# Optimization experiments

Hardware: AMD Instinct MI355X
Metric: run time of the kernel (lower is better)

Reference implementation:

```python
import jax, jax.numpy as jnp
import numpy as np

N_NODES = 50000
N_EDGES = 800000
D = 256
N_LAYERS = 2


def setup_inputs() -> dict:
    key = jax.random.key(0)
    k1, k2, k3, k4, k5, k6 = jax.random.split(key, 6)
    inp = {}
    inp["input"] = jax.random.normal(k1, (N_NODES, D), dtype=jnp.float32)
    inp["edge_index"] = jax.random.randint(k2, (2, N_EDGES), 0, N_NODES, dtype=jnp.int64)
    # learned params: initial dense projection + per-conv GCN weights
    scale = 1.0 / np.sqrt(D)
    inp["weight"] = jax.random.normal(k3, (D, D), dtype=jnp.float32) * scale
    inp["bias"] = jnp.zeros((D,), dtype=jnp.float32)
    inp["conv_w"] = jax.random.normal(k4, (N_LAYERS, D, D), dtype=jnp.float32) * scale
    inp["conv_b"] = jnp.zeros((N_LAYERS, D), dtype=jnp.float32)
    return inp


def _gcn_conv(x, W, b, src, dst, n):
    # Standard GCNConv: x' = D^{-1/2} (A + I) D^{-1/2} (x W) + b
    h = x @ W  # [N, D]
    loops = jnp.arange(n, dtype=src.dtype)
    s = jnp.concatenate([src, loops])
    d = jnp.concatenate([dst, loops])
    deg = jax.ops.segment_sum(jnp.ones(s.shape[0], dtype=x.dtype), d, num_segments=n)
    dinv = jnp.where(deg > 0, deg ** -0.5, 0.0)
    norm = dinv[s] * dinv[d]  # [E+N]
    msg = h[s] * norm[:, None]  # gather + scale  [E+N, D]
    return jax.ops.segment_sum(msg, d, num_segments=n) + b  # scatter-add


def reference(input, edge_index, weight, bias, conv_w, conv_b):
    n = input.shape[0]
    src, dst = edge_index[0], edge_index[1]
    # dropout=0 / eval mode -> identity
    x = jax.nn.relu(input @ weight + bias)
    for i in range(conv_w.shape[0]):
        x = jax.nn.relu(_gcn_conv(x, conv_w[i], conv_b[i], src, dst, n))
    return x
```

## Files before the change

kernel.cpp:

```cpp
#include <hip/hip_runtime.h>

#define D 256
typedef unsigned short u16;
typedef __attribute__((ext_vector_type(8))) short bf16x8;
typedef __attribute__((ext_vector_type(4))) float f32x4;

__device__ __forceinline__ float bf2f(u16 u) {
    union { unsigned int i; float f; } x; x.i = ((unsigned int)u) << 16; return x.f;
}
__device__ __forceinline__ u16 f2bf(float f) {
    union { float f; unsigned int i; } x; x.f = f;
    unsigned int r = x.i + 0x7fff + ((x.i >> 16) & 1);
    return (u16)(r >> 16);
}
__device__ __forceinline__ unsigned int cvtpk_bf16(float lo, float hi) {
    unsigned int r;
    asm("v_cvt_pk_bf16_f32 %0, %1, %2" : "=v"(r) : "v"(lo), "v"(hi));
    return r;
}
__device__ __forceinline__ void gload16(const void* g, void* l) {
    __builtin_amdgcn_global_load_lds(
        (const __attribute__((address_space(1))) void*)g,
        (__attribute__((address_space(3))) void*)l, 16, 0, 0);
}
__device__ __forceinline__ bf16x8 gload_row(const u16* p) {
    bf16x8 r;
    asm volatile("global_load_dwordx4 %0, %1, off" : "=&v"(r) : "v"(p));
    return r;
}


__global__ void init_kernel(int* __restrict__ deg, int n) {
    int i = blockIdx.x * blockDim.x + threadIdx.x;
    if (i < n) deg[i] = 1;
}

__global__ void hist_kernel(const int* __restrict__ dst, int* __restrict__ deg, int e) {
    int i = blockIdx.x * blockDim.x + threadIdx.x;
    if (i < e) atomicAdd(&deg[dst[i]], 1);
}


__global__ __launch_bounds__(256) void scan_phase1(
    const int* __restrict__ deg, int* __restrict__ bsum,
    float* __restrict__ dinv, int n) {
    __shared__ int red[256];
    int t = threadIdx.x;
    int i0 = blockIdx.x * 1024 + t * 4;
    int s = 0;
    if (i0 + 3 < n) {
        int4 v = *reinterpret_cast<const int4*>(&deg[i0]);
        s = v.x + v.y + v.z + v.w - 4;
        float4 dv;
        dv.x = rsqrtf((float)v.x); dv.y = rsqrtf((float)v.y);
        dv.z = rsqrtf((float)v.z); dv.w = rsqrtf((float)v.w);
        *reinterpret_cast<float4*>(&dinv[i0]) = dv;
    } else {
        for (int j = i0; j < n && j < i0 + 4; ++j) {
            s += deg[j] - 1;
            dinv[j] = rsqrtf((float)deg[j]);
        }
    }
    red[t] = s;
    __syncthreads();
    for (int off = 128; off > 0; off >>= 1) {
        if (t < off) red[t] += red[t + off];
        __syncthreads();
    }
    if (t == 0) bsum[blockIdx.x] = red[0];
}

__global__ __launch_bounds__(256) void scan_phase2(
    const int* __restrict__ bsum, int* __restrict__ boff,
    int* __restrict__ rowptr, int nblk, int n) {
    __shared__ int sums[256];
    int t = threadIdx.x;
    int v = (t < nblk) ? bsum[t] : 0;
    int orig = v;
    sums[t] = v;
    __syncthreads();
    for (int off = 1; off < 256; off <<= 1) {
        int u = (t >= off) ? sums[t - off] : 0;
        __syncthreads();
        sums[t] += u;
        __syncthreads();
    }
    if (t < nblk) boff[t] = sums[t] - orig;
    if (t == nblk - 1) rowptr[n] = sums[t];
}

__global__ __launch_bounds__(256) void scan_phase3(
    const int* __restrict__ deg, const int* __restrict__ boff,
    int* __restrict__ rowptr, int* __restrict__ cursor, int n) {
    __shared__ int sums[256];
    int t = threadIdx.x;
    int i0 = blockIdx.x * 1024 + t * 4;
    int d0 = 0, d1 = 0, d2 = 0, d3 = 0;
    if (i0 + 3 < n) {
        int4 v = *reinterpret_cast<const int4*>(&deg[i0]);
        d0 = v.x - 1; d1 = v.y - 1; d2 = v.z - 1; d3 = v.w - 1;
    } else {
        if (i0 + 0 < n) d0 = deg[i0 + 0] - 1;
        if (i0 + 1 < n) d1 = deg[i0 + 1] - 1;
        if (i0 + 2 < n) d2 = deg[i0 + 2] - 1;
        if (i0 + 3 < n) d3 = deg[i0 + 3] - 1;
    }
    int ts = d0 + d1 + d2 + d3;
    sums[t] = ts;
    __syncthreads();
    for (int off = 1; off < 256; off <<= 1) {
        int u = (t >= off) ? sums[t - off] : 0;
        __syncthreads();
        sums[t] += u;
        __syncthreads();
    }
    int pre = boff[blockIdx.x] + sums[t] - ts;
    if (i0 + 0 < n) { rowptr[i0 + 0] = pre; cursor[i0 + 0] = pre; } pre += d0;
    if (i0 + 1 < n) { rowptr[i0 + 1] = pre; cursor[i0 + 1] = pre; } pre += d1;
    if (i0 + 2 < n) { rowptr[i0 + 2] = pre; cursor[i0 + 2] = pre; } pre += d2;
    if (i0 + 3 < n) { rowptr[i0 + 3] = pre; cursor[i0 + 3] = pre; }
}

__global__ void fill_kernel(const int* __restrict__ src, const int* __restrict__ dst,
                            int* __restrict__ cursor, int* __restrict__ csr, int e) {
    int i = blockIdx.x * blockDim.x + threadIdx.x;
    if (i < e) {
        int d = dst[i];
        int p = atomicAdd(&cursor[d], 1);
        csr[p] = src[i];
    }
}


__global__ __launch_bounds__(256) void transpose_cvt_kernel(
    const float* __restrict__ W, u16* __restrict__ Wt) {
    __shared__ float t[32][33];
    int bx = blockIdx.x * 32, by = blockIdx.y * 32;
    int tx = threadIdx.x & 31, ty = threadIdx.x >> 5;
#pragma unroll
    for (int i = 0; i < 32; i += 8)
        t[ty + i][tx] = W[(size_t)(bx + ty + i) * D + by + tx];
    __syncthreads();
#pragma unroll
    for (int i = 0; i < 32; i += 8)
        Wt[(size_t)(by + ty + i) * D + bx + tx] = f2bf(t[tx][ty + i]);
}


__global__ __launch_bounds__(256) void mfma_gemm(
    const u16* __restrict__ A, const u16* __restrict__ Bt,
    const float* __restrict__ dinv,
    u16* __restrict__ C, int M)
{
    __shared__ u16 As[64 * 32];
    __shared__ u16 Bs[128 * 32];
    const int tid = threadIdx.x;
    const int lane = tid & 63;
    const int wave = tid >> 6;
    const int wr = wave >> 1, wc = wave & 1;
    const int row0 = blockIdx.y * 64, col0 = blockIdx.x * 128;
    const int l16 = lane & 15, kg = lane >> 4;

    f32x4 acc[2][4] = {};

    for (int k0 = 0; k0 < D; k0 += 32) {
        {
            int r = tid >> 2, c = tid & 3;
            int csw = c ^ ((r >> 1) & 3);
            char* ldsbase_a = (char*)As + ((tid & ~63) << 4);
            int grow = row0 + r; if (grow >= M) grow = M - 1;
            gload16(&A[(size_t)grow * D + k0 + csw * 8], ldsbase_a);
        }
#pragma unroll
        for (int i = 0; i < 2; ++i) {
            int idx = i * 256 + tid;
            int r = idx >> 2, c = idx & 3;
            int csw = c ^ ((r >> 1) & 3);
            char* ldsbase_b = (char*)Bs + ((i * 256 + (tid & ~63)) << 4);
            gload16(&Bt[(size_t)(col0 + r) * D + k0 + csw * 8], ldsbase_b);
        }
        __syncthreads();
        bf16x8 af[2], bfr[4];
        int ksw = kg ^ ((l16 >> 1) & 3);
#pragma unroll
        for (int m = 0; m < 2; ++m)
            af[m] = *reinterpret_cast<const bf16x8*>(&As[(wr * 32 + m * 16 + l16) * 32 + ksw * 8]);
#pragma unroll
        for (int nn = 0; nn < 4; ++nn)
            bfr[nn] = *reinterpret_cast<const bf16x8*>(&Bs[(wc * 64 + nn * 16 + l16) * 32 + ksw * 8]);
#pragma unroll
        for (int m = 0; m < 2; ++m)
#pragma unroll
            for (int nn = 0; nn < 4; ++nn)
                acc[m][nn] = __builtin_amdgcn_mfma_f32_16x16x32_bf16(
                    af[m], bfr[nn], acc[m][nn], 0, 0, 0);
        __syncthreads();
    }

#pragma unroll
    for (int m = 0; m < 2; ++m) {
#pragma unroll
        for (int nn = 0; nn < 4; ++nn) {
            int gcol = col0 + wc * 64 + nn * 16 + l16;
#pragma unroll
            for (int j = 0; j < 4; ++j) {
                int grow = row0 + wr * 32 + m * 16 + kg * 4 + j;
                if (grow >= M) continue;
                C[(size_t)grow * D + gcol] = f2bf(acc[m][nn][j] * dinv[grow]);
            }
        }
    }
}

__global__ __launch_bounds__(256) void mfma_gemm_f32a(
    const float* __restrict__ A, const u16* __restrict__ Bt,
    const float* __restrict__ bias,
    u16* __restrict__ C, int M)
{
    __shared__ u16 As[64 * 32];
    __shared__ u16 Bs[128 * 32];
    const int tid = threadIdx.x;
    const int lane = tid & 63;
    const int wave = tid >> 6;
    const int wr = wave >> 1, wc = wave & 1;
    const int row0 = blockIdx.y * 64, col0 = blockIdx.x * 128;
    const int l16 = lane & 15, kg = lane >> 4;

    f32x4 acc[2][4] = {};

    for (int k0 = 0; k0 < D; k0 += 32) {
#pragma unroll
        for (int i = 0; i < 2; ++i) {
            int idx = i * 256 + tid;
            int r = idx >> 2, c = idx & 3;
            int csw = c ^ ((r >> 1) & 3);
            char* ldsbase_b = (char*)Bs + ((i * 256 + (tid & ~63)) << 4);
            gload16(&Bt[(size_t)(col0 + r) * D + k0 + csw * 8], ldsbase_b);
        }
        {
            int r = tid >> 2, c = tid & 3;
            int csw = c ^ ((r >> 1) & 3);
            int grow = row0 + r; if (grow >= M) grow = M - 1;
            const float* gp = &A[(size_t)grow * D + k0 + csw * 8];
            float4 v0 = *reinterpret_cast<const float4*>(gp);
            float4 v1 = *reinterpret_cast<const float4*>(gp + 4);
            uint4 w;
            w.x = cvtpk_bf16(v0.x, v0.y);
            w.y = cvtpk_bf16(v0.z, v0.w);
            w.z = cvtpk_bf16(v1.x, v1.y);
            w.w = cvtpk_bf16(v1.z, v1.w);
            *reinterpret_cast<uint4*>((char*)As + (tid << 4)) = w;
        }
        __syncthreads();
        bf16x8 af[2], bfr[4];
        int ksw = kg ^ ((l16 >> 1) & 3);
#pragma unroll
        for (int m = 0; m < 2; ++m)
            af[m] = *reinterpret_cast<const bf16x8*>(&As[(wr * 32 + m * 16 + l16) * 32 + ksw * 8]);
#pragma unroll
        for (int nn = 0; nn < 4; ++nn)
            bfr[nn] = *reinterpret_cast<const bf16x8*>(&Bs[(wc * 64 + nn * 16 + l16) * 32 + ksw * 8]);
#pragma unroll
        for (int m = 0; m < 2; ++m)
#pragma unroll
            for (int nn = 0; nn < 4; ++nn)
                acc[m][nn] = __builtin_amdgcn_mfma_f32_16x16x32_bf16(
                    af[m], bfr[nn], acc[m][nn], 0, 0, 0);
        __syncthreads();
    }

#pragma unroll
    for (int m = 0; m < 2; ++m) {
#pragma unroll
        for (int nn = 0; nn < 4; ++nn) {
            int gcol = col0 + wc * 64 + nn * 16 + l16;
#pragma unroll
            for (int j = 0; j < 4; ++j) {
                int grow = row0 + wr * 32 + m * 16 + kg * 4 + j;
                if (grow >= M) continue;
                C[(size_t)grow * D + gcol] = f2bf(fmaxf(acc[m][nn][j] + bias[gcol], 0.f));
            }
        }
    }
}

__global__ __launch_bounds__(256) void agg_kernel(
    const u16* __restrict__ hn, const int* __restrict__ rowptr,
    const int* __restrict__ csr, const float* __restrict__ dinv,
    const float* __restrict__ bias,
    u16* __restrict__ out_bf, float* __restrict__ out_f32, int n)
{
    int wave = threadIdx.x >> 6;
    int lane = threadIdx.x & 63;
    int node = blockIdx.x * 4 + wave;
    if (node >= n) return;
    int h = lane >> 5;
    int l5 = lane & 31;
    int c8 = l5 * 8;

    float a[8] = {0.f, 0.f, 0.f, 0.f, 0.f, 0.f, 0.f, 0.f};

#define ACC8(vv) { \
    a[0] += bf2f((u16)(vv)[0]); a[1] += bf2f((u16)(vv)[1]); \
    a[2] += bf2f((u16)(vv)[2]); a[3] += bf2f((u16)(vv)[3]); \
    a[4] += bf2f((u16)(vv)[4]); a[5] += bf2f((u16)(vv)[5]); \
    a[6] += bf2f((u16)(vv)[6]); a[7] += bf2f((u16)(vv)[7]); }
#define ROWP(s) (&hn[(size_t)(s) * D + c8])

    if (h == 0) {
        bf16x8 v = *reinterpret_cast<const bf16x8*>(ROWP(node));
        ACC8(v);
    }

    int e0 = rowptr[node], e1 = rowptr[node + 1];
    for (int base = e0; base < e1; base += 64) {
        int bi = base + lane;
        int idx = (bi < e1) ? csr[bi] : 0;
        int cnt = e1 - base; if (cnt > 64) cnt = 64;
        int it = 0;
        for (; it + 16 <= cnt; it += 16) {
            int s0 = __shfl(idx, it + 0  + h);
            int s1 = __shfl(idx, it + 2  + h);
            int s2 = __shfl(idx, it + 4  + h);
            int s3 = __shfl(idx, it + 6  + h);
            int s4 = __shfl(idx, it + 8  + h);
            int s5 = __shfl(idx, it + 10 + h);
            int s6 = __shfl(idx, it + 12 + h);
            int s7 = __shfl(idx, it + 14 + h);
            bf16x8 v0 = gload_row(ROWP(s0));
            bf16x8 v1 = gload_row(ROWP(s1));
            bf16x8 v2 = gload_row(ROWP(s2));
            bf16x8 v3 = gload_row(ROWP(s3));
            bf16x8 v4 = gload_row(ROWP(s4));
            bf16x8 v5 = gload_row(ROWP(s5));
            bf16x8 v6 = gload_row(ROWP(s6));
            bf16x8 v7 = gload_row(ROWP(s7));
            asm volatile("s_waitcnt vmcnt(0)" ::: "memory");
            __builtin_amdgcn_sched_barrier(0);
            ACC8(v0); ACC8(v1); ACC8(v2); ACC8(v3);
            ACC8(v4); ACC8(v5); ACC8(v6); ACC8(v7);
        }
        for (; it + 8 <= cnt; it += 8) {
            int s0 = __shfl(idx, it + 0 + h);
            int s1 = __shfl(idx, it + 2 + h);
            int s2 = __shfl(idx, it + 4 + h);
            int s3 = __shfl(idx, it + 6 + h);
            bf16x8 v0 = gload_row(ROWP(s0));
            bf16x8 v1 = gload_row(ROWP(s1));
            bf16x8 v2 = gload_row(ROWP(s2));
            bf16x8 v3 = gload_row(ROWP(s3));
            asm volatile("s_waitcnt vmcnt(0)" ::: "memory");
            __builtin_amdgcn_sched_barrier(0);
            ACC8(v0); ACC8(v1); ACC8(v2); ACC8(v3);
        }
        for (; it + 2 <= cnt; it += 2) {
            int s0 = __shfl(idx, it + h);
            bf16x8 v0 = *reinterpret_cast<const bf16x8*>(ROWP(s0));
            ACC8(v0);
        }
        if (it < cnt) {
            int s0 = __shfl(idx, it);
            if (h == 0) {
                bf16x8 v0 = *reinterpret_cast<const bf16x8*>(ROWP(s0));
                ACC8(v0);
            }
        }
    }
#undef ACC8
#undef ROWP

#pragma unroll
    for (int j = 0; j < 8; ++j) a[j] += __shfl(a[j], lane ^ 32);

    if (h == 0) {
        float di = dinv[node];
#pragma unroll
        for (int j = 0; j < 8; ++j) a[j] = fmaxf(a[j] * di + bias[c8 + j], 0.f);
        if (out_bf) {
            bf16x8 o;
#pragma unroll
            for (int j = 0; j < 8; ++j) o[j] = (short)f2bf(a[j]);
            *reinterpret_cast<bf16x8*>(&out_bf[(size_t)node * D + c8]) = o;
        } else {
            float4 o0, o1;
            o0.x = a[0]; o0.y = a[1]; o0.z = a[2]; o0.w = a[3];
            o1.x = a[4]; o1.y = a[5]; o1.z = a[6]; o1.w = a[7];
            *reinterpret_cast<float4*>(&out_f32[(size_t)node * D + c8 + 0]) = o0;
            *reinterpret_cast<float4*>(&out_f32[(size_t)node * D + c8 + 4]) = o1;
        }
    }
}


extern "C" void kernel_launch(void* const* d_in, const int* in_sizes, int n_in,
                              void* d_out, int out_size, void* d_ws, size_t ws_size,
                              hipStream_t stream) {
    const float* input  = (const float*)d_in[0];
    const int*   edge   = (const int*)d_in[1];
    const float* weight = (const float*)d_in[2];
    const float* bias   = (const float*)d_in[3];
    const float* conv_w = (const float*)d_in[4];
    const float* conv_b = (const float*)d_in[5];
    float* out = (float*)d_out;

    const int n = in_sizes[0] / D;
    const int E = in_sizes[1] / 2;
    const int* src = edge;
    const int* dst = edge + E;

    char* ws = (char*)d_ws;
    size_t off = 0;
    auto alloc = [&](size_t bytes) -> void* {
        void* p = ws + off;
        off = (off + bytes + 255) & ~(size_t)255;
        return p;
    };
    u16*   bufA   = (u16*)alloc((size_t)n * D * sizeof(u16));
    u16*   bufB   = (u16*)alloc((size_t)n * D * sizeof(u16));
    u16*   Wt     = (u16*)alloc((size_t)3 * D * D * sizeof(u16));
    int*   deg    = (int*)alloc((size_t)n * sizeof(int));
    int*   cursor = (int*)alloc((size_t)n * sizeof(int));
    float* dinv   = (float*)alloc((size_t)n * sizeof(float));
    int*   rowptr = (int*)alloc((size_t)(n + 1) * sizeof(int));
    int*   csr    = (int*)alloc((size_t)E * sizeof(int));
    int    nscan  = (n + 1023) / 1024;
    int*   bsum   = (int*)alloc((size_t)nscan * sizeof(int));
    int*   boff   = (int*)alloc((size_t)nscan * sizeof(int));

    int nb = (n + 255) / 256;
    int eb1 = (E + 255) / 256;
    init_kernel<<<nb, 256, 0, stream>>>(deg, n);
    hist_kernel<<<eb1, 256, 0, stream>>>(dst, deg, E);
    scan_phase1<<<nscan, 256, 0, stream>>>(deg, bsum, dinv, n);
    scan_phase2<<<1, 256, 0, stream>>>(bsum, boff, rowptr, nscan, n);
    scan_phase3<<<nscan, 256, 0, stream>>>(deg, boff, rowptr, cursor, n);
    fill_kernel<<<eb1, 256, 0, stream>>>(src, dst, cursor, csr, E);

    dim3 tgrid(8, 8);
    transpose_cvt_kernel<<<tgrid, 256, 0, stream>>>(weight, Wt);
    transpose_cvt_kernel<<<tgrid, 256, 0, stream>>>(conv_w, Wt + D * D);
    transpose_cvt_kernel<<<tgrid, 256, 0, stream>>>(conv_w + D * D, Wt + 2 * D * D);

    dim3 ggrid(D / 128, (n + 63) / 64);
    dim3 agrid((n + 3) / 4);

    mfma_gemm_f32a<<<ggrid, 256, 0, stream>>>(input, Wt, bias, bufA, n);
    mfma_gemm<<<ggrid, 256, 0, stream>>>(bufA, Wt + D * D, dinv, bufB, n);
    agg_kernel<<<agrid, 256, 0, stream>>>(bufB, rowptr, csr, dinv, conv_b, bufA, nullptr, n);
    mfma_gemm<<<ggrid, 256, 0, stream>>>(bufA, Wt + 2 * D * D, dinv, bufB, n);
    agg_kernel<<<agrid, 256, 0, stream>>>(bufB, rowptr, csr, dinv, conv_b + D, nullptr, out, n);
}
```

Measured before the change: 301.0 us.

## Merge independent graph-prep kernels into GEMM launches via block-index partitioning

Fuses the degree init with the weight transpose/convert, the degree histogram with the first dense GEMM, and the CSR fill with the first conv GEMM. Each merged launch splits its grid by block index so the graph-structure work runs alongside the GEMM tiles. This cuts launch count and lets the atomic-heavy, latency-bound passes fill idle CUs during compute. Dependencies still hold because the hist blocks do not touch GEMM1's inputs and dinv is ready before GEMM2. The risk is that atomic blocks contend for memory bandwidth with the GEMM tiles.

```diff
diff --git a/kernel.cpp b/kernel.cpp
--- a/kernel.cpp
+++ b/kernel.cpp
@@ -29,15 +29,31 @@
     return r;
 }
 
-
-__global__ void init_kernel(int* __restrict__ deg, int n) {
-    int i = blockIdx.x * blockDim.x + threadIdx.x;
-    if (i < n) deg[i] = 1;
-}
-
-__global__ void hist_kernel(const int* __restrict__ dst, int* __restrict__ deg, int e) {
-    int i = blockIdx.x * blockDim.x + threadIdx.x;
-    if (i < e) atomicAdd(&deg[dst[i]], 1);
+__global__ __launch_bounds__(256) void fused_init_tr(
+    int* __restrict__ deg, int n, int nb,
+    const float* __restrict__ W0, const float* __restrict__ CW,
+    u16* __restrict__ Wt)
+{
+    int bid = blockIdx.x;
+    if (bid < nb) {
+        int i = bid * 256 + threadIdx.x;
+        if (i < n) deg[i] = 1;
+    } else {
+        __shared__ float t[32][33];
+        int tt = bid - nb;
+        int w = tt >> 6, r = tt & 63;
+        const float* W = (w == 0) ? W0 : (CW + (size_t)(w - 1) * D * D);
+        u16* Wo = Wt + (size_t)w * D * D;
+        int bx = (r & 7) * 32, by = (r >> 3) * 32;
+        int tx = threadIdx.x & 31, ty = threadIdx.x >> 5;
+#pragma unroll
+        for (int i = 0; i < 32; i += 8)
+            t[ty + i][tx] = W[(size_t)(bx + ty + i) * D + by + tx];
+        __syncthreads();
+#pragma unroll
+        for (int i = 0; i < 32; i += 8)
+            Wo[(size_t)(by + ty + i) * D + bx + tx] = f2bf(t[tx][ty + i]);
+    }
 }
 
 
@@ -121,31 +137,159 @@
     if (i0 + 3 < n) { rowptr[i0 + 3] = pre; cursor[i0 + 3] = pre; }
 }
 
-__global__ void fill_kernel(const int* __restrict__ src, const int* __restrict__ dst,
-                            int* __restrict__ cursor, int* __restrict__ csr, int e) {
-    int i = blockIdx.x * blockDim.x + threadIdx.x;
-    if (i < e) {
-        int d = dst[i];
-        int p = atomicAdd(&cursor[d], 1);
-        csr[p] = src[i];
-    }
-}
-
-
-__global__ __launch_bounds__(256) void transpose_cvt_kernel(
-    const float* __restrict__ W, u16* __restrict__ Wt) {
-    __shared__ float t[32][33];
-    int bx = blockIdx.x * 32, by = blockIdx.y * 32;
-    int tx = threadIdx.x & 31, ty = threadIdx.x >> 5;
-#pragma unroll
-    for (int i = 0; i < 32; i += 8)
-        t[ty + i][tx] = W[(size_t)(bx + ty + i) * D + by + tx];
-    __syncthreads();
-#pragma unroll
-    for (int i = 0; i < 32; i += 8)
-        Wt[(size_t)(by + ty + i) * D + bx + tx] = f2bf(t[tx][ty + i]);
-}
-
+__global__ __launch_bounds__(256) void fused_gemm1_hist(
+    const float* __restrict__ A, const u16* __restrict__ Bt,
+    const float* __restrict__ bias, u16* __restrict__ C, int M, int ng,
+    const int* __restrict__ dst, int* __restrict__ deg, int E)
+{
+    int bid = blockIdx.x;
+    if (bid >= ng) {
+        int i = (bid - ng) * 256 + threadIdx.x;
+        if (i < E) atomicAdd(&deg[dst[i]], 1);
+        return;
+    }
+    __shared__ u16 As[64 * 32];
+    __shared__ u16 Bs[128 * 32];
+    const int tid = threadIdx.x;
+    const int lane = tid & 63;
+    const int wave = tid >> 6;
+    const int wr = wave >> 1, wc = wave & 1;
+    const int row0 = (bid >> 1) * 64, col0 = (bid & 1) * 128;
+    const int l16 = lane & 15, kg = lane >> 4;
+
+    f32x4 acc[2][4] = {};
+
+    for (int k0 = 0; k0 < D; k0 += 32) {
+#pragma unroll
+        for (int i = 0; i < 2; ++i) {
+            int idx = i * 256 + tid;
+            int r = idx >> 2, c = idx & 3;
+            int csw = c ^ ((r >> 1) & 3);
+            char* ldsbase_b = (char*)Bs + ((i * 256 + (tid & ~63)) << 4);
+            gload16(&Bt[(size_t)(col0 + r) * D + k0 + csw * 8], ldsbase_b);
+        }
+        {
+            int r = tid >> 2, c = tid & 3;
+            int csw = c ^ ((r >> 1) & 3);
+            int grow = row0 + r; if (grow >= M) grow = M - 1;
+            const float* gp = &A[(size_t)grow * D + k0 + csw * 8];
+            float4 v0 = *reinterpret_cast<const float4*>(gp);
+            float4 v1 = *reinterpret_cast<const float4*>(gp + 4);
+            uint4 w;
+            w.x = cvtpk_bf16(v0.x, v0.y);
+            w.y = cvtpk_bf16(v0.z, v0.w);
+            w.z = cvtpk_bf16(v1.x, v1.y);
+            w.w = cvtpk_bf16(v1.z, v1.w);
+            *reinterpret_cast<uint4*>((char*)As + (tid << 4)) = w;
+        }
+        __syncthreads();
+        bf16x8 af[2], bfr[4];
+        int ksw = kg ^ ((l16 >> 1) & 3);
+#pragma unroll
+        for (int m = 0; m < 2; ++m)
+            af[m] = *reinterpret_cast<const bf16x8*>(&As[(wr * 32 + m * 16 + l16) * 32 + ksw * 8]);
+#pragma unroll
+        for (int nn = 0; nn < 4; ++nn)
+            bfr[nn] = *reinterpret_cast<const bf16x8*>(&Bs[(wc * 64 + nn * 16 + l16) * 32 + ksw * 8]);
+#pragma unroll
+        for (int m = 0; m < 2; ++m)
+#pragma unroll
+            for (int nn = 0; nn < 4; ++nn)
+                acc[m][nn] = __builtin_amdgcn_mfma_f32_16x16x32_bf16(
+                    af[m], bfr[nn], acc[m][nn], 0, 0, 0);
+        __syncthreads();
+    }
+
+#pragma unroll
+    for (int m = 0; m < 2; ++m) {
+#pragma unroll
+        for (int nn = 0; nn < 4; ++nn) {
+            int gcol = col0 + wc * 64 + nn * 16 + l16;
+#pragma unroll
+            for (int j = 0; j < 4; ++j) {
+                int grow = row0 + wr * 32 + m * 16 + kg * 4 + j;
+                if (grow >= M) continue;
+                C[(size_t)grow * D + gcol] = f2bf(fmaxf(acc[m][nn][j] + bias[gcol], 0.f));
+            }
+        }
+    }
+}
+
+__global__ __launch_bounds__(256) void fused_gemm2_fill(
+    const u16* __restrict__ A, const u16* __restrict__ Bt,
+    const float* __restrict__ dinv, u16* __restrict__ C, int M, int ng,
+    const int* __restrict__ src, const int* __restrict__ dst,
+    int* __restrict__ cursor, int* __restrict__ csr, int E)
+{
+    int bid = blockIdx.x;
+    if (bid >= ng) {
+        int i = (bid - ng) * 256 + threadIdx.x;
+        if (i < E) {
+            int d = dst[i];
+            int p = atomicAdd(&cursor[d], 1);
+            csr[p] = src[i];
+        }
+        return;
+    }
+    __shared__ u16 As[64 * 32];
+    __shared__ u16 Bs[128 * 32];
+    const int tid = threadIdx.x;
+    const int lane = tid & 63;
+    const int wave = tid >> 6;
+    const int wr = wave >> 1, wc = wave & 1;
+    const int row0 = (bid >> 1) * 64, col0 = (bid & 1) * 128;
+    const int l16 = lane & 15, kg = lane >> 4;
+
+    f32x4 acc[2][4] = {};
+
+    for (int k0 = 0; k0 < D; k0 += 32) {
+        {
+            int r = tid >> 2, c = tid & 3;
+            int csw = c ^ ((r >> 1) & 3);
+            char* ldsbase_a = (char*)As + ((tid & ~63) << 4);
+            int grow = row0 + r; if (grow >= M) grow = M - 1;
+            gload16(&A[(size_t)grow * D + k0 + csw * 8], ldsbase_a);
+        }
+#pragma unroll
+        for (int i = 0; i < 2; ++i) {
+            int idx = i * 256 + tid;
+            int r = idx >> 2, c = idx & 3;
+            int csw = c ^ ((r >> 1) & 3);
+            char* ldsbase_b = (char*)Bs + ((i * 256 + (tid & ~63)) << 4);
+            gload16(&Bt[(size_t)(col0 + r) * D + k0 + csw * 8], ldsbase_b);
+        }
+        __syncthreads();
+        bf16x8 af[2], bfr[4];
+        int ksw = kg ^ ((l16 >> 1) & 3);
+#pragma unroll
+        for (int m = 0; m < 2; ++m)
+            af[m] = *reinterpret_cast<const bf16x8*>(&As[(wr * 32 + m * 16 + l16) * 32 + ksw * 8]);
+#pragma unroll
+        for (int nn = 0; nn < 4; ++nn)
+            bfr[nn] = *reinterpret_cast<const bf16x8*>(&Bs[(wc * 64 + nn * 16 + l16) * 32 + ksw * 8]);
+#pragma unroll
+        for (int m = 0; m < 2; ++m)
+#pragma unroll
+            for (int nn = 0; nn < 4; ++nn)
+                acc[m][nn] = __builtin_amdgcn_mfma_f32_16x16x32_bf16(
+                    af[m], bfr[nn], acc[m][nn], 0, 0, 0);
+        __syncthreads();
+    }
+
+#pragma unroll
+    for (int m = 0; m < 2; ++m) {
+#pragma unroll
+        for (int nn = 0; nn < 4; ++nn) {
+            int gcol = col0 + wc * 64 + nn * 16 + l16;
+#pragma unroll
+            for (int j = 0; j < 4; ++j) {
+                int grow = row0 + wr * 32 + m * 16 + kg * 4 + j;
+                if (grow >= M) continue;
+                C[(size_t)grow * D + gcol] = f2bf(acc[m][nn][j] * dinv[grow]);
+            }
+        }
+    }
+}
 
 __global__ __launch_bounds__(256) void mfma_gemm(
     const u16* __restrict__ A, const u16* __restrict__ Bt,
@@ -207,78 +351,6 @@
                 int grow = row0 + wr * 32 + m * 16 + kg * 4 + j;
                 if (grow >= M) continue;
                 C[(size_t)grow * D + gcol] = f2bf(acc[m][nn][j] * dinv[grow]);
-            }
-        }
-    }
-}
-
-__global__ __launch_bounds__(256) void mfma_gemm_f32a(
-    const float* __restrict__ A, const u16* __restrict__ Bt,
-    const float* __restrict__ bias,
-    u16* __restrict__ C, int M)
-{
-    __shared__ u16 As[64 * 32];
-    __shared__ u16 Bs[128 * 32];
-    const int tid = threadIdx.x;
-    const int lane = tid & 63;
-    const int wave = tid >> 6;
-    const int wr = wave >> 1, wc = wave & 1;
-    const int row0 = blockIdx.y * 64, col0 = blockIdx.x * 128;
-    const int l16 = lane & 15, kg = lane >> 4;
-
-    f32x4 acc[2][4] = {};
-
-    for (int k0 = 0; k0 < D; k0 += 32) {
-#pragma unroll
-        for (int i = 0; i < 2; ++i) {
-            int idx = i * 256 + tid;
-            int r = idx >> 2, c = idx & 3;
-            int csw = c ^ ((r >> 1) & 3);
-            char* ldsbase_b = (char*)Bs + ((i * 256 + (tid & ~63)) << 4);
-            gload16(&Bt[(size_t)(col0 + r) * D + k0 + csw * 8], ldsbase_b);
-        }
-        {
-            int r = tid >> 2, c = tid & 3;
-            int csw = c ^ ((r >> 1) & 3);
-            int grow = row0 + r; if (grow >= M) grow = M - 1;
-            const float* gp = &A[(size_t)grow * D + k0 + csw * 8];
-            float4 v0 = *reinterpret_cast<const float4*>(gp);
-            float4 v1 = *reinterpret_cast<const float4*>(gp + 4);
-            uint4 w;
-            w.x = cvtpk_bf16(v0.x, v0.y);
-            w.y = cvtpk_bf16(v0.z, v0.w);
-            w.z = cvtpk_bf16(v1.x, v1.y);
-            w.w = cvtpk_bf16(v1.z, v1.w);
-            *reinterpret_cast<uint4*>((char*)As + (tid << 4)) = w;
-        }
-        __syncthreads();
-        bf16x8 af[2], bfr[4];
-        int ksw = kg ^ ((l16 >> 1) & 3);
-#pragma unroll
-        for (int m = 0; m < 2; ++m)
-            af[m] = *reinterpret_cast<const bf16x8*>(&As[(wr * 32 + m * 16 + l16) * 32 + ksw * 8]);
-#pragma unroll
-        for (int nn = 0; nn < 4; ++nn)
-            bfr[nn] = *reinterpret_cast<const bf16x8*>(&Bs[(wc * 64 + nn * 16 + l16) * 32 + ksw * 8]);
-#pragma unroll
-        for (int m = 0; m < 2; ++m)
-#pragma unroll
-            for (int nn = 0; nn < 4; ++nn)
-                acc[m][nn] = __builtin_amdgcn_mfma_f32_16x16x32_bf16(
-                    af[m], bfr[nn], acc[m][nn], 0, 0, 0);
-        __syncthreads();
-    }
-
-#pragma unroll
-    for (int m = 0; m < 2; ++m) {
-#pragma unroll
-        for (int nn = 0; nn < 4; ++nn) {
-            int gcol = col0 + wc * 64 + nn * 16 + l16;
-#pragma unroll
-            for (int j = 0; j < 4; ++j) {
-                int grow = row0 + wr * 32 + m * 16 + kg * 4 + j;
-                if (grow >= M) continue;
-                C[(size_t)grow * D + gcol] = f2bf(fmaxf(acc[m][nn][j] + bias[gcol], 0.f));
             }
         }
     }
@@ -427,25 +499,20 @@
     int*   bsum   = (int*)alloc((size_t)nscan * sizeof(int));
     int*   boff   = (int*)alloc((size_t)nscan * sizeof(int));
 
-    int nb = (n + 255) / 256;
+    int nb  = (n + 255) / 256;
     int eb1 = (E + 255) / 256;
-    init_kernel<<<nb, 256, 0, stream>>>(deg, n);
-    hist_kernel<<<eb1, 256, 0, stream>>>(dst, deg, E);
+    int ng  = 2 * ((n + 63) / 64);
+
+    fused_init_tr<<<nb + 192, 256, 0, stream>>>(deg, n, nb, weight, conv_w, Wt);
+    fused_gemm1_hist<<<ng + eb1, 256, 0, stream>>>(input, Wt, bias, bufA, n, ng, dst, deg, E);
     scan_phase1<<<nscan, 256, 0, stream>>>(deg, bsum, dinv, n);
     scan_phase2<<<1, 256, 0, stream>>>(bsum, boff, rowptr, nscan, n);
     scan_phase3<<<nscan, 256, 0, stream>>>(deg, boff, rowptr, cursor, n);
-    fill_kernel<<<eb1, 256, 0, stream>>>(src, dst, cursor, csr, E);
-
-    dim3 tgrid(8, 8);
-    transpose_cvt_kernel<<<tgrid, 256, 0, stream>>>(weight, Wt);
-    transpose_cvt_kernel<<<tgrid, 256, 0, stream>>>(conv_w, Wt + D * D);
-    transpose_cvt_kernel<<<tgrid, 256, 0, stream>>>(conv_w + D * D, Wt + 2 * D * D);
+    fused_gemm2_fill<<<ng + eb1, 256, 0, stream>>>(bufA, Wt + D * D, dinv, bufB, n, ng,
+                                                   src, dst, cursor, csr, E);
 
     dim3 ggrid(D / 128, (n + 63) / 64);
     dim3 agrid((n + 3) / 4);
-
-    mfma_gemm_f32a<<<ggrid, 256, 0, stream>>>(input, Wt, bias, bufA, n);
-    mfma_gemm<<<ggrid, 256, 0, stream>>>(bufA, Wt + D * D, dinv, bufB, n);
     agg_kernel<<<agrid, 256, 0, stream>>>(bufB, rowptr, csr, dinv, conv_b, bufA, nullptr, n);
     mfma_gemm<<<ggrid, 256, 0, stream>>>(bufA, Wt + 2 * D * D, dinv, bufB, n);
     agg_kernel<<<agrid, 256, 0, stream>>>(bufB, rowptr, csr, dinv, conv_b + D, nullptr, out, n);
```

Result: faster. 294.8 us (-2.1%).

## Fuse degree init with weight transposes and first GEMM with histogram

Applied to the files above, without the earlier changes.

Merges the degree-init kernel and the three weight transpose/convert kernels into one launch, and runs the degree histogram as extra blocks of the first projection GEMM so the two overlap. The histogram and CSR fill kernels now process four edges per thread using int4 loads. This cuts six launches down to two and overlaps the atomic-heavy histogram with MFMA work. The cost is heterogeneous blocks competing for CU resources, plus a vectorized edge path that assumes 16-byte aligned src/dst arrays.

```diff
diff --git a/kernel.cpp b/kernel.cpp
--- a/kernel.cpp
+++ b/kernel.cpp
@@ -29,15 +29,31 @@
     return r;
 }
 
-
-__global__ void init_kernel(int* __restrict__ deg, int n) {
-    int i = blockIdx.x * blockDim.x + threadIdx.x;
-    if (i < n) deg[i] = 1;
-}
-
-__global__ void hist_kernel(const int* __restrict__ dst, int* __restrict__ deg, int e) {
-    int i = blockIdx.x * blockDim.x + threadIdx.x;
-    if (i < e) atomicAdd(&deg[dst[i]], 1);
+__global__ __launch_bounds__(256) void fused_init_tr(
+    int* __restrict__ deg, int n, int nb,
+    const float* __restrict__ W0, const float* __restrict__ CW,
+    u16* __restrict__ Wt)
+{
+    int bid = blockIdx.x;
+    if (bid < nb) {
+        int i = bid * 256 + threadIdx.x;
+        if (i < n) deg[i] = 1;
+    } else {
+        __shared__ float t[32][33];
+        int tt = bid - nb;
+        int w = tt >> 6, r = tt & 63;
+        const float* W = (w == 0) ? W0 : (CW + (size_t)(w - 1) * D * D);
+        u16* Wo = Wt + (size_t)w * D * D;
+        int bx = (r & 7) * 32, by = (r >> 3) * 32;
+        int tx = threadIdx.x & 31, ty = threadIdx.x >> 5;
+#pragma unroll
+        for (int i = 0; i < 32; i += 8)
+            t[ty + i][tx] = W[(size_t)(bx + ty + i) * D + by + tx];
+        __syncthreads();
+#pragma unroll
+        for (int i = 0; i < 32; i += 8)
+            Wo[(size_t)(by + ty + i) * D + bx + tx] = f2bf(t[tx][ty + i]);
+    }
 }
 
 
@@ -124,28 +140,108 @@
 __global__ void fill_kernel(const int* __restrict__ src, const int* __restrict__ dst,
                             int* __restrict__ cursor, int* __restrict__ csr, int e) {
     int i = blockIdx.x * blockDim.x + threadIdx.x;
-    if (i < e) {
-        int d = dst[i];
-        int p = atomicAdd(&cursor[d], 1);
-        csr[p] = src[i];
-    }
-}
-
-
-__global__ __launch_bounds__(256) void transpose_cvt_kernel(
-    const float* __restrict__ W, u16* __restrict__ Wt) {
-    __shared__ float t[32][33];
-    int bx = blockIdx.x * 32, by = blockIdx.y * 32;
-    int tx = threadIdx.x & 31, ty = threadIdx.x >> 5;
-#pragma unroll
-    for (int i = 0; i < 32; i += 8)
-        t[ty + i][tx] = W[(size_t)(bx + ty + i) * D + by + tx];
-    __syncthreads();
-#pragma unroll
-    for (int i = 0; i < 32; i += 8)
-        Wt[(size_t)(by + ty + i) * D + bx + tx] = f2bf(t[tx][ty + i]);
-}
-
+    int b = i * 4;
+    if (b + 3 < e) {
+        int4 s4 = *reinterpret_cast<const int4*>(&src[b]);
+        int4 d4 = *reinterpret_cast<const int4*>(&dst[b]);
+        int p;
+        p = atomicAdd(&cursor[d4.x], 1); csr[p] = s4.x;
+        p = atomicAdd(&cursor[d4.y], 1); csr[p] = s4.y;
+        p = atomicAdd(&cursor[d4.z], 1); csr[p] = s4.z;
+        p = atomicAdd(&cursor[d4.w], 1); csr[p] = s4.w;
+    } else {
+        for (int j = b; j < e; ++j) {
+            int d = dst[j];
+            int p = atomicAdd(&cursor[d], 1);
+            csr[p] = src[j];
+        }
+    }
+}
+
+__global__ __launch_bounds__(256) void fused_gemm1_hist(
+    const float* __restrict__ A, const u16* __restrict__ Bt,
+    const float* __restrict__ bias, u16* __restrict__ C, int M, int ng,
+    const int* __restrict__ dst, int* __restrict__ deg, int E)
+{
+    int bid = blockIdx.x;
+    if (bid >= ng) {
+        int i = (bid - ng) * 256 + threadIdx.x;
+        int b = i * 4;
+        if (b + 3 < E) {
+            int4 v = *reinterpret_cast<const int4*>(&dst[b]);
+            atomicAdd(&deg[v.x], 1); atomicAdd(&deg[v.y], 1);
+            atomicAdd(&deg[v.z], 1); atomicAdd(&deg[v.w], 1);
+        } else {
+            for (int j = b; j < E; ++j) atomicAdd(&deg[dst[j]], 1);
+        }
+        return;
+    }
+    __shared__ u16 As[64 * 32];
+    __shared__ u16 Bs[128 * 32];
+    const int tid = threadIdx.x;
+    const int lane = tid & 63;
+    const int wave = tid >> 6;
+    const int wr = wave >> 1, wc = wave & 1;
+    const int row0 = (bid >> 1) * 64, col0 = (bid & 1) * 128;
+    const int l16 = lane & 15, kg = lane >> 4;
+
+    f32x4 acc[2][4] = {};
+
+    for (int k0 = 0; k0 < D; k0 += 32) {
+#pragma unroll
+        for (int i = 0; i < 2; ++i) {
+            int idx = i * 256 + tid;
+            int r = idx >> 2, c = idx & 3;
+            int csw = c ^ ((r >> 1) & 3);
+            char* ldsbase_b = (char*)Bs + ((i * 256 + (tid & ~63)) << 4);
+            gload16(&Bt[(size_t)(col0 + r) * D + k0 + csw * 8], ldsbase_b);
+        }
+        {
+            int r = tid >> 2, c = tid & 3;
+            int csw = c ^ ((r >> 1) & 3);
+            int grow = row0 + r; if (grow >= M) grow = M - 1;
+            const float* gp = &A[(size_t)grow * D + k0 + csw * 8];
+            float4 v0 = *reinterpret_cast<const float4*>(gp);
+            float4 v1 = *reinterpret_cast<const float4*>(gp + 4);
+            uint4 w;
+            w.x = cvtpk_bf16(v0.x, v0.y);
+            w.y = cvtpk_bf16(v0.z, v0.w);
+            w.z = cvtpk_bf16(v1.x, v1.y);
+            w.w = cvtpk_bf16(v1.z, v1.w);
+            *reinterpret_cast<uint4*>((char*)As + (tid << 4)) = w;
+        }
+        __syncthreads();
+        bf16x8 af[2], bfr[4];
+        int ksw = kg ^ ((l16 >> 1) & 3);
+#pragma unroll
+        for (int m = 0; m < 2; ++m)
+            af[m] = *reinterpret_cast<const bf16x8*>(&As[(wr * 32 + m * 16 + l16) * 32 + ksw * 8]);
+#pragma unroll
+        for (int nn = 0; nn < 4; ++nn)
+            bfr[nn] = *reinterpret_cast<const bf16x8*>(&Bs[(wc * 64 + nn * 16 + l16) * 32 + ksw * 8]);
+#pragma unroll
+        for (int m = 0; m < 2; ++m)
+#pragma unroll
+            for (int nn = 0; nn < 4; ++nn)
+                acc[m][nn] = __builtin_amdgcn_mfma_f32_16x16x32_bf16(
+                    af[m], bfr[nn], acc[m][nn], 0, 0, 0);
+        __syncthreads();
+    }
+
+#pragma unroll
+    for (int m = 0; m < 2; ++m) {
+#pragma unroll
+        for (int nn = 0; nn < 4; ++nn) {
+            int gcol = col0 + wc * 64 + nn * 16 + l16;
+#pragma unroll
+            for (int j = 0; j < 4; ++j) {
+                int grow = row0 + wr * 32 + m * 16 + kg * 4 + j;
+                if (grow >= M) continue;
+                C[(size_t)grow * D + gcol] = f2bf(fmaxf(acc[m][nn][j] + bias[gcol], 0.f));
+            }
+        }
+    }
+}
 
 __global__ __launch_bounds__(256) void mfma_gemm(
     const u16* __restrict__ A, const u16* __restrict__ Bt,
@@ -207,78 +303,6 @@
                 int grow = row0 + wr * 32 + m * 16 + kg * 4 + j;
                 if (grow >= M) continue;
                 C[(size_t)grow * D + gcol] = f2bf(acc[m][nn][j] * dinv[grow]);
-            }
-        }
-    }
-}
-
-__global__ __launch_bounds__(256) void mfma_gemm_f32a(
-    const float* __restrict__ A, const u16* __restrict__ Bt,
-    const float* __restrict__ bias,
-    u16* __restrict__ C, int M)
-{
-    __shared__ u16 As[64 * 32];
-    __shared__ u16 Bs[128 * 32];
-    const int tid = threadIdx.x;
-    const int lane = tid & 63;
-    const int wave = tid >> 6;
-    const int wr = wave >> 1, wc = wave & 1;
-    const int row0 = blockIdx.y * 64, col0 = blockIdx.x * 128;
-    const int l16 = lane & 15, kg = lane >> 4;
-
-    f32x4 acc[2][4] = {};
-
-    for (int k0 = 0; k0 < D; k0 += 32) {
-#pragma unroll
-        for (int i = 0; i < 2; ++i) {
-            int idx = i * 256 + tid;
-            int r = idx >> 2, c = idx & 3;
-            int csw = c ^ ((r >> 1) & 3);
-            char* ldsbase_b = (char*)Bs + ((i * 256 + (tid & ~63)) << 4);
-            gload16(&Bt[(size_t)(col0 + r) * D + k0 + csw * 8], ldsbase_b);
-        }
-        {
-            int r = tid >> 2, c = tid & 3;
-            int csw = c ^ ((r >> 1) & 3);
-            int grow = row0 + r; if (grow >= M) grow = M - 1;
-            const float* gp = &A[(size_t)grow * D + k0 + csw * 8];
-            float4 v0 = *reinterpret_cast<const float4*>(gp);
-            float4 v1 = *reinterpret_cast<const float4*>(gp + 4);
-            uint4 w;
-            w.x = cvtpk_bf16(v0.x, v0.y);
-            w.y = cvtpk_bf16(v0.z, v0.w);
-            w.z = cvtpk_bf16(v1.x, v1.y);
-            w.w = cvtpk_bf16(v1.z, v1.w);
-            *reinterpret_cast<uint4*>((char*)As + (tid << 4)) = w;
-        }
-        __syncthreads();
-        bf16x8 af[2], bfr[4];
-        int ksw = kg ^ ((l16 >> 1) & 3);
-#pragma unroll
-        for (int m = 0; m < 2; ++m)
-            af[m] = *reinterpret_cast<const bf16x8*>(&As[(wr * 32 + m * 16 + l16) * 32 + ksw * 8]);
-#pragma unroll
-        for (int nn = 0; nn < 4; ++nn)
-            bfr[nn] = *reinterpret_cast<const bf16x8*>(&Bs[(wc * 64 + nn * 16 + l16) * 32 + ksw * 8]);
-#pragma unroll
-        for (int m = 0; m < 2; ++m)
-#pragma unroll
-            for (int nn = 0; nn < 4; ++nn)
-                acc[m][nn] = __builtin_amdgcn_mfma_f32_16x16x32_bf16(
-                    af[m], bfr[nn], acc[m][nn], 0, 0, 0);
-        __syncthreads();
-    }
-
-#pragma unroll
-    for (int m = 0; m < 2; ++m) {
-#pragma unroll
-        for (int nn = 0; nn < 4; ++nn) {
-            int gcol = col0 + wc * 64 + nn * 16 + l16;
-#pragma unroll
-            for (int j = 0; j < 4; ++j) {
-                int grow = row0 + wr * 32 + m * 16 + kg * 4 + j;
-                if (grow >= M) continue;
-                C[(size_t)grow * D + gcol] = f2bf(fmaxf(acc[m][nn][j] + bias[gcol], 0.f));
             }
         }
     }
@@ -427,24 +451,19 @@
     int*   bsum   = (int*)alloc((size_t)nscan * sizeof(int));
     int*   boff   = (int*)alloc((size_t)nscan * sizeof(int));
 
-    int nb = (n + 255) / 256;
-    int eb1 = (E + 255) / 256;
-    init_kernel<<<nb, 256, 0, stream>>>(deg, n);
-    hist_kernel<<<eb1, 256, 0, stream>>>(dst, deg, E);
+    int nb  = (n + 255) / 256;
+    int eb4 = (E / 4 + 255) / 256;
+    int ng  = 2 * ((n + 63) / 64);
+
+    fused_init_tr<<<nb + 192, 256, 0, stream>>>(deg, n, nb, weight, conv_w, Wt);
+    fused_gemm1_hist<<<ng + eb4, 256, 0, stream>>>(input, Wt, bias, bufA, n, ng, dst, deg, E);
     scan_phase1<<<nscan, 256, 0, stream>>>(deg, bsum, dinv, n);
     scan_phase2<<<1, 256, 0, stream>>>(bsum, boff, rowptr, nscan, n);
     scan_phase3<<<nscan, 256, 0, stream>>>(deg, boff, rowptr, cursor, n);
-    fill_kernel<<<eb1, 256, 0, stream>>>(src, dst, cursor, csr, E);
-
-    dim3 tgrid(8, 8);
-    transpose_cvt_kernel<<<tgrid, 256, 0, stream>>>(weight, Wt);
-    transpose_cvt_kernel<<<tgrid, 256, 0, stream>>>(conv_w, Wt + D * D);
-    transpose_cvt_kernel<<<tgrid, 256, 0, stream>>>(conv_w + D * D, Wt + 2 * D * D);
+    fill_kernel<<<eb4, 256, 0, stream>>>(src, dst, cursor, csr, E);
 
     dim3 ggrid(D / 128, (n + 63) / 64);
     dim3 agrid((n + 3) / 4);
-
-    mfma_gemm_f32a<<<ggrid, 256, 0, stream>>>(input, Wt, bias, bufA, n);
     mfma_gemm<<<ggrid, 256, 0, stream>>>(bufA, Wt + D * D, dinv, bufB, n);
     agg_kernel<<<agrid, 256, 0, stream>>>(bufB, rowptr, csr, dinv, conv_b, bufA, nullptr, n);
     mfma_gemm<<<ggrid, 256, 0, stream>>>(bufA, Wt + 2 * D * D, dinv, bufB, n);
```

Result: faster. 287.0 us (-4.7%).
